# Kernel tuning notes

Hardware: AMD Instinct MI355X
Metric: run time of the kernel (lower is better)

Reference implementation:

```python
import jax, jax.numpy as jnp
import numpy as np

B, C, H, W, L = 2, 64, 48, 48, 48
GH, GW, GL = 24, 24, 24  # gating signal at half resolution


def setup_inputs() -> dict:
    key = jax.random.key(0)
    k = jax.random.split(key, 6)
    x = jax.random.normal(k[0], (B, C, H, W, L), dtype=jnp.float32)
    g = jax.random.normal(k[1], (B, C, GH, GW, GL), dtype=jnp.float32)
    s = 1.0 / np.sqrt(C)
    W1 = jax.random.normal(k[2], (C, C), dtype=jnp.float32) * s  # conv1 1x1x1 weight (out,in)
    b1 = jax.random.normal(k[3], (C,), dtype=jnp.float32) * 0.01
    W2 = jax.random.normal(k[4], (C, C), dtype=jnp.float32) * s  # conv2 1x1x1 weight
    b2 = jax.random.normal(k[5], (C,), dtype=jnp.float32) * 0.01
    return {"x": x, "g": g, "W1": W1, "b1": b1, "W2": W2, "b2": b2}


def _conv1x1(v, Wm, b):
    # 1x1x1 Conv3d == channel-mixing matmul
    return jnp.einsum('bchwl,oc->bohwl', v, Wm) + b[None, :, None, None, None]


def reference(x, g, W1, b1, W2, b2):
    theta_x = _conv1x1(x, W1, b1)                       # (B, C, H, W, L)
    theta_g = _conv1x1(g, W2, b2)                       # (B, C, GH, GW, GL)
    # F.upsample(mode='trilinear', align_corners=False) -> half-pixel trilinear resize
    theta_g = jax.image.resize(theta_g, (B, C, H, W, L), method='trilinear')

    # spatially-normalized elementwise gate
    theta_c = theta_x * theta_g
    theta_c = theta_c - jnp.min(theta_c)                # global min over whole tensor
    theta_c = theta_c / jnp.sum(theta_c, axis=(2, 3, 4), keepdims=True)
    p = theta_c * x

    # channel-channel attention per (b,h,w), contracting over L
    theta_c_d = jnp.einsum('bihwl,bjhwl->bhwij', theta_x, theta_g)  # (B,H,W,C,C)
    theta_c_d = theta_c_d - jnp.min(theta_c_d)
    theta_c_d = theta_c_d / jnp.sum(theta_c_d, axis=(1, 2, 3, 4), keepdims=True)
    d = jnp.einsum('bchwl,bhwcj->bjhwl', x, theta_c_d)  # (B, C, H, W, L)
    return (p, d)
```

## Files before the change

### kernel.cpp

```cpp
#include <hip/hip_runtime.h>

#define Bb 2
#define Cc 64
#define Hh 48
#define Ww 48
#define Ll 48
#define HWc (Hh*Ww)
#define HWL (HWc*Ll)
#define GHh 24
#define SG (GHh*GHh*GHh)
#define NBLK (Bb*HWc)
#define CNT1f 110592.0f
#define CNT2f 9437184.0f

__device__ __forceinline__ void interp1(int i, int& a, int& b, float& f){
  float src = i*0.5f - 0.25f;
  float fl = floorf(src);
  f = src - fl;
  int i0 = (int)fl;
  a = i0 < 0 ? 0 : i0;
  int i1 = i0 + 1;
  b = i1 > (GHh-1) ? (GHh-1) : i1;
}

__global__ __launch_bounds__(256) void conv_k(const float* __restrict__ in,
    const float* __restrict__ Wm, const float* __restrict__ bias,
    float* __restrict__ out, int S){
  __shared__ __align__(16) float Wl[64][68];
  __shared__ __align__(16) float xl[64][68];
  int t = threadIdx.x;
  int ntile = S >> 6;
  int b  = blockIdx.x / ntile;
  int s0 = (blockIdx.x % ntile) << 6;
  for (int q = t; q < 4096; q += 256){
    int o = q >> 6, c = q & 63;
    Wl[c][o] = Wm[q];
  }
  const float* inb = in + (size_t)b*Cc*S + s0;
  for (int q = t; q < 1024; q += 256){
    int c = q >> 4, v = (q & 15) << 2;
    float4 val = *(const float4*)(inb + (size_t)c*S + v);
    *(float4*)&xl[c][v] = val;
  }
  __syncthreads();
  int o0 = (t & 15) << 2, s1 = (t >> 4) << 2;
  float a00=0,a01=0,a02=0,a03=0,a10=0,a11=0,a12=0,a13=0;
  float a20=0,a21=0,a22=0,a23=0,a30=0,a31=0,a32=0,a33=0;
  #pragma unroll 8
  for (int c = 0; c < 64; ++c){
    float4 wv = *(const float4*)&Wl[c][o0];
    float4 xv = *(const float4*)&xl[c][s1];
    a00 += wv.x*xv.x; a01 += wv.x*xv.y; a02 += wv.x*xv.z; a03 += wv.x*xv.w;
    a10 += wv.y*xv.x; a11 += wv.y*xv.y; a12 += wv.y*xv.z; a13 += wv.y*xv.w;
    a20 += wv.z*xv.x; a21 += wv.z*xv.y; a22 += wv.z*xv.z; a23 += wv.z*xv.w;
    a30 += wv.w*xv.x; a31 += wv.w*xv.y; a32 += wv.w*xv.z; a33 += wv.w*xv.w;
  }
  float* ob = out + (size_t)b*Cc*S + s0 + s1;
  float b0 = bias[o0+0], b1v = bias[o0+1], b2v = bias[o0+2], b3 = bias[o0+3];
  { float4 r = make_float4(a00+b0,a01+b0,a02+b0,a03+b0); *(float4*)(ob + (size_t)(o0+0)*S) = r; }
  { float4 r = make_float4(a10+b1v,a11+b1v,a12+b1v,a13+b1v); *(float4*)(ob + (size_t)(o0+1)*S) = r; }
  { float4 r = make_float4(a20+b2v,a21+b2v,a22+b2v,a23+b2v); *(float4*)(ob + (size_t)(o0+2)*S) = r; }
  { float4 r = make_float4(a30+b3,a31+b3,a32+b3,a33+b3); *(float4*)(ob + (size_t)(o0+3)*S) = r; }
}

__global__ __launch_bounds__(256) void reduce_k(const float* __restrict__ tx,
    const float* __restrict__ tgh, float* __restrict__ tgsite,
    float* __restrict__ part_row, float* __restrict__ pm1,
    float* __restrict__ pm2, float* __restrict__ ps2){
  __shared__ __align__(16) float txt[64*52];
  __shared__ __align__(16) float tgt[64*52];
  __shared__ float Msh[64*25];
  __shared__ float red[512];
  __shared__ float sxg[48];
  int t = threadIdx.x;
  int bIdx = blockIdx.x;
  int b = bIdx / HWc, hw = bIdx % HWc;
  int h = hw / Ww, w = hw % Ww;
  int ha, hb; float fh; interp1(h, ha, hb, fh);
  int wa, wb; float fw; interp1(w, wa, wb, fw);
  float omh = 1.f - fh, omw = 1.f - fw;
  const float* txb = tx + ((size_t)b*Cc*HWc + hw)*Ll;
  #pragma unroll
  for (int k = 0; k < 3; ++k){
    int q = t + (k << 8);
    int c = q / 12, v = (q % 12) << 2;
    *(float4*)&txt[c*52+v] = *(const float4*)(txb + (size_t)c*HWL + v);
  }
  const float* gb = tgh + (size_t)b*Cc*SG;
  #pragma unroll
  for (int k = 0; k < 6; ++k){
    int q = t + (k << 8);
    int c = q / 24, j = q % 24;
    const float* gc = gb + (size_t)c*SG;
    float vaa = gc[ha*576 + wa*24 + j];
    float vba = gc[hb*576 + wa*24 + j];
    float vab = gc[ha*576 + wb*24 + j];
    float vbb = gc[hb*576 + wb*24 + j];
    float mwa = omh*vaa + fh*vba;
    float mwb = omh*vab + fh*vbb;
    Msh[c*25 + j] = omw*mwa + fw*mwb;
  }
  __syncthreads();
  float* tgs = tgsite + (size_t)bIdx*3072;
  #pragma unroll
  for (int k = 0; k < 3; ++k){
    int q = t + (k << 8);
    int c = q / 12, l4 = (q % 12) << 2;
    float4 r;
    float* rp = &r.x;
    #pragma unroll
    for (int i = 0; i < 4; ++i){
      int l = l4 + i;
      int la, lb; float fl; interp1(l, la, lb, fl);
      rp[i] = (1.f-fl)*Msh[c*25+la] + fl*Msh[c*25+lb];
    }
    *(float4*)&tgt[c*52+l4] = r;
    *(float4*)(tgs + c*48 + l4) = r;
  }
  __syncthreads();
  int c = t & 63, lq = t >> 6;
  float psum = 0.f, pmin = 3.4e38f;
  #pragma unroll
  for (int m = 0; m < 3; ++m){
    int l4 = (lq << 2) + (m << 4);
    float4 a = *(const float4*)&txt[c*52+l4];
    float4 g = *(const float4*)&tgt[c*52+l4];
    float p0 = a.x*g.x, p1 = a.y*g.y, p2 = a.z*g.z, p3 = a.w*g.w;
    psum += p0+p1+p2+p3;
    pmin = fminf(pmin, fminf(fminf(p0,p1), fminf(p2,p3)));
  }
  red[t] = psum;
  if (t < 48){
    float sx = 0.f, sg = 0.f;
    #pragma unroll 8
    for (int cc = 0; cc < 64; ++cc){ sx += txt[cc*52+t]; sg += tgt[cc*52+t]; }
    sxg[t] = sx*sg;
  }
  int i0 = (t & 15) << 2, j0 = (t >> 4) << 2;
  float a00=0,a01=0,a02=0,a03=0,a10=0,a11=0,a12=0,a13=0;
  float a20=0,a21=0,a22=0,a23=0,a30=0,a31=0,a32=0,a33=0;
  #pragma unroll 4
  for (int l0 = 0; l0 < 48; l0 += 4){
    float4 x0 = *(const float4*)&txt[(i0+0)*52 + l0];
    float4 x1 = *(const float4*)&txt[(i0+1)*52 + l0];
    float4 x2 = *(const float4*)&txt[(i0+2)*52 + l0];
    float4 x3 = *(const float4*)&txt[(i0+3)*52 + l0];
    float4 g0 = *(const float4*)&tgt[(j0+0)*52 + l0];
    float4 g1 = *(const float4*)&tgt[(j0+1)*52 + l0];
    float4 g2 = *(const float4*)&tgt[(j0+2)*52 + l0];
    float4 g3 = *(const float4*)&tgt[(j0+3)*52 + l0];
    a00 += x0.x*g0.x + x0.y*g0.y + x0.z*g0.z + x0.w*g0.w;
    a01 += x0.x*g1.x + x0.y*g1.y + x0.z*g1.z + x0.w*g1.w;
    a02 += x0.x*g2.x + x0.y*g2.y + x0.z*g2.z + x0.w*g2.w;
    a03 += x0.x*g3.x + x0.y*g3.y + x0.z*g3.z + x0.w*g3.w;
    a10 += x1.x*g0.x + x1.y*g0.y + x1.z*g0.z + x1.w*g0.w;
    a11 += x1.x*g1.x + x1.y*g1.y + x1.z*g1.z + x1.w*g1.w;
    a12 += x1.x*g2.x + x1.y*g2.y + x1.z*g2.z + x1.w*g2.w;
    a13 += x1.x*g3.x + x1.y*g3.y + x1.z*g3.z + x1.w*g3.w;
    a20 += x2.x*g0.x + x2.y*g0.y + x2.z*g0.z + x2.w*g0.w;
    a21 += x2.x*g1.x + x2.y*g1.y + x2.z*g1.z + x2.w*g1.w;
    a22 += x2.x*g2.x + x2.y*g2.y + x2.z*g2.z + x2.w*g2.w;
    a23 += x2.x*g3.x + x2.y*g3.y + x2.z*g3.z + x2.w*g3.w;
    a30 += x3.x*g0.x + x3.y*g0.y + x3.z*g0.z + x3.w*g0.w;
    a31 += x3.x*g1.x + x3.y*g1.y + x3.z*g1.z + x3.w*g1.w;
    a32 += x3.x*g2.x + x3.y*g2.y + x3.z*g2.z + x3.w*g2.w;
    a33 += x3.x*g3.x + x3.y*g3.y + x3.z*g3.z + x3.w*g3.w;
  }
  float amin = fminf(fminf(fminf(a00,a01),fminf(a02,a03)),
               fminf(fminf(fminf(a10,a11),fminf(a12,a13)),
               fminf(fminf(fminf(a20,a21),fminf(a22,a23)),
                     fminf(fminf(a30,a31),fminf(a32,a33)))));
  __syncthreads();
  if (t < 64) part_row[(size_t)bIdx*64 + t] = red[t]+red[t+64]+red[t+128]+red[t+192];
  __syncthreads();
  red[t] = pmin; red[256+t] = amin;
  __syncthreads();
  if (t < 128){
    red[t] = fminf(red[t], red[t+128]);
    red[256+t] = fminf(red[256+t], red[384+t]);
  }
  __syncthreads();
  if (t < 64){
    float v1 = fminf(red[t], red[t+64]);
    float v2 = fminf(red[256+t], red[320+t]);
    #pragma unroll
    for (int off = 32; off; off >>= 1){
      v1 = fminf(v1, __shfl_down(v1, off));
      v2 = fminf(v2, __shfl_down(v2, off));
    }
    if (t == 0){
      pm1[bIdx] = v1; pm2[bIdx] = v2;
      float tot = 0.f;
      #pragma unroll
      for (int l = 0; l < 48; ++l) tot += sxg[l];
      ps2[bIdx] = tot;
    }
  }
}

__global__ __launch_bounds__(256) void reduce2_k(const float* __restrict__ part_row,
    const float* __restrict__ pm1, const float* __restrict__ pm2,
    const float* __restrict__ ps2, float* __restrict__ rowsum,
    float* __restrict__ gmin, float* __restrict__ s2v){
  __shared__ float red[512];
  int t = threadIdx.x, blk = blockIdx.x;
  if (blk < 128){
    int b = blk >> 6, c = blk & 63;
    const float* src = part_row + (size_t)b*HWc*64 + c;
    float s = 0.f;
    #pragma unroll
    for (int k = 0; k < 9; ++k){
      int i = t + (k << 8);
      s += src[(size_t)i*64];
    }
    red[t] = s; __syncthreads();
    for (int sgap = 128; sgap >= 64; sgap >>= 1){
      if (t < sgap) red[t] += red[t+sgap];
      __syncthreads();
    }
    if (t < 64){
      float v = red[t];
      #pragma unroll
      for (int off = 32; off; off >>= 1) v += __shfl_down(v, off);
      if (t == 0) rowsum[blk] = v;
    }
  } else if (blk == 128){
    float m1 = 3.4e38f, m2 = 3.4e38f;
    for (int i = t; i < NBLK; i += 256){ m1 = fminf(m1, pm1[i]); m2 = fminf(m2, pm2[i]); }
    red[t] = m1; red[256+t] = m2; __syncthreads();
    for (int s = 128; s >= 1; s >>= 1){
      if (t < s){ red[t] = fminf(red[t], red[t+s]); red[256+t] = fminf(red[256+t], red[256+t+s]); }
      __syncthreads();
    }
    if (t == 0){ gmin[0] = red[0]; gmin[1] = red[256]; }
  } else {
    float sa = 0.f, sb = 0.f;
    for (int i = t; i < HWc; i += 256){ sa += ps2[i]; sb += ps2[HWc + i]; }
    red[t] = sa; red[256+t] = sb; __syncthreads();
    for (int s = 128; s >= 1; s >>= 1){
      if (t < s){ red[t] += red[t+s]; red[256+t] += red[256+t+s]; }
      __syncthreads();
    }
    if (t == 0){ s2v[0] = red[0]; s2v[1] = red[256]; }
  }
}

__global__ __launch_bounds__(256) void final_k(const float* __restrict__ x,
    const float* __restrict__ tx, const float* __restrict__ tgsite,
    const float* __restrict__ gmin, const float* __restrict__ rowsum,
    const float* __restrict__ s2v, float* __restrict__ outp, float* __restrict__ outd){
  __shared__ __align__(16) float txt[64*52];
  __shared__ __align__(16) float tgt[64*52];
  __shared__ __align__(16) float xs[64*52];
  __shared__ float iv1[64];
  int t = threadIdx.x;
  int bIdx = blockIdx.x;
  int b = bIdx / HWc, hw = bIdx % HWc;
  size_t sbase = ((size_t)b*Cc*HWc + hw)*Ll;
  const float* txb = tx + sbase;
  const float* xb  = x  + sbase;
  const float* tgs = tgsite + (size_t)bIdx*3072;
  float m1 = gmin[0], m2 = gmin[1];
  #pragma unroll
  for (int k = 0; k < 3; ++k){
    int q = t + (k << 8);
    int c = q / 12, v = (q % 12) << 2;
    *(float4*)&txt[c*52+v] = *(const float4*)(txb + (size_t)c*HWL + v);
    *(float4*)&xs [c*52+v] = *(const float4*)(xb  + (size_t)c*HWL + v);
    *(float4*)&tgt[c*52+v] = *(const float4*)(tgs + (q << 2));
  }
  if (t < 64) iv1[t] = 1.f/(rowsum[b*64 + t] - m1*CNT1f);
  float invd2 = 1.f/(s2v[b] - m2*CNT2f);
  __syncthreads();
  int i0 = (t & 15) << 2, j0 = (t >> 4) << 2;
  float a00=0,a01=0,a02=0,a03=0,a10=0,a11=0,a12=0,a13=0;
  float a20=0,a21=0,a22=0,a23=0,a30=0,a31=0,a32=0,a33=0;
  #pragma unroll 4
  for (int l0 = 0; l0 < 48; l0 += 4){
    float4 x0 = *(const float4*)&txt[(i0+0)*52 + l0];
    float4 x1 = *(const float4*)&txt[(i0+1)*52 + l0];
    float4 x2 = *(const float4*)&txt[(i0+2)*52 + l0];
    float4 x3 = *(const float4*)&txt[(i0+3)*52 + l0];
    float4 g0 = *(const float4*)&tgt[(j0+0)*52 + l0];
    float4 g1 = *(const float4*)&tgt[(j0+1)*52 + l0];
    float4 g2 = *(const float4*)&tgt[(j0+2)*52 + l0];
    float4 g3 = *(const float4*)&tgt[(j0+3)*52 + l0];
    a00 += x0.x*g0.x + x0.y*g0.y + x0.z*g0.z + x0.w*g0.w;
    a01 += x0.x*g1.x + x0.y*g1.y + x0.z*g1.z + x0.w*g1.w;
    a02 += x0.x*g2.x + x0.y*g2.y + x0.z*g2.z + x0.w*g2.w;
    a03 += x0.x*g3.x + x0.y*g3.y + x0.z*g3.z + x0.w*g3.w;
    a10 += x1.x*g0.x + x1.y*g0.y + x1.z*g0.z + x1.w*g0.w;
    a11 += x1.x*g1.x + x1.y*g1.y + x1.z*g1.z + x1.w*g1.w;
    a12 += x1.x*g2.x + x1.y*g2.y + x1.z*g2.z + x1.w*g2.w;
    a13 += x1.x*g3.x + x1.y*g3.y + x1.z*g3.z + x1.w*g3.w;
    a20 += x2.x*g0.x + x2.y*g0.y + x2.z*g0.z + x2.w*g0.w;
    a21 += x2.x*g1.x + x2.y*g1.y + x2.z*g1.z + x2.w*g1.w;
    a22 += x2.x*g2.x + x2.y*g2.y + x2.z*g2.z + x2.w*g2.w;
    a23 += x2.x*g3.x + x2.y*g3.y + x2.z*g3.z + x2.w*g3.w;
    a30 += x3.x*g0.x + x3.y*g0.y + x3.z*g0.z + x3.w*g0.w;
    a31 += x3.x*g1.x + x3.y*g1.y + x3.z*g1.z + x3.w*g1.w;
    a32 += x3.x*g2.x + x3.y*g2.y + x3.z*g2.z + x3.w*g2.w;
    a33 += x3.x*g3.x + x3.y*g3.y + x3.z*g3.z + x3.w*g3.w;
  }
  #pragma unroll
  for (int k = 0; k < 3; ++k){
    int q = t + (k << 8);
    int c = q / 12, l4 = (q % 12) << 2;
    float4 a = *(const float4*)&txt[c*52+l4];
    float4 g = *(const float4*)&tgt[c*52+l4];
    float4 xv = *(const float4*)&xs[c*52+l4];
    float s = iv1[c];
    float4 r = make_float4((a.x*g.x - m1)*s*xv.x, (a.y*g.y - m1)*s*xv.y,
                           (a.z*g.z - m1)*s*xv.z, (a.w*g.w - m1)*s*xv.w);
    *(float4*)(outp + sbase + (size_t)c*HWL + l4) = r;
  }
  __syncthreads();
  float* At = txt;
  { float4 r = make_float4((a00-m2)*invd2,(a01-m2)*invd2,(a02-m2)*invd2,(a03-m2)*invd2);
    *(float4*)&At[(i0+0)*52 + j0] = r; }
  { float4 r = make_float4((a10-m2)*invd2,(a11-m2)*invd2,(a12-m2)*invd2,(a13-m2)*invd2);
    *(float4*)&At[(i0+1)*52 + j0] = r; }
  { float4 r = make_float4((a20-m2)*invd2,(a21-m2)*invd2,(a22-m2)*invd2,(a23-m2)*invd2);
    *(float4*)&At[(i0+2)*52 + j0] = r; }
  { float4 r = make_float4((a30-m2)*invd2,(a31-m2)*invd2,(a32-m2)*invd2,(a33-m2)*invd2);
    *(float4*)&At[(i0+3)*52 + j0] = r; }
  __syncthreads();
  if (t < 192){
    int jj = (t & 15) << 2, l0 = (t >> 4) << 2;
    float d00=0,d01=0,d02=0,d03=0,d10=0,d11=0,d12=0,d13=0;
    float d20=0,d21=0,d22=0,d23=0,d30=0,d31=0,d32=0,d33=0;
    #pragma unroll 4
    for (int cc = 0; cc < 64; ++cc){
      float4 av = *(const float4*)&At[cc*52 + jj];
      float4 xv = *(const float4*)&xs[cc*52 + l0];
      d00 += av.x*xv.x; d01 += av.x*xv.y; d02 += av.x*xv.z; d03 += av.x*xv.w;
      d10 += av.y*xv.x; d11 += av.y*xv.y; d12 += av.y*xv.z; d13 += av.y*xv.w;
      d20 += av.z*xv.x; d21 += av.z*xv.y; d22 += av.z*xv.z; d23 += av.z*xv.w;
      d30 += av.w*xv.x; d31 += av.w*xv.y; d32 += av.w*xv.z; d33 += av.w*xv.w;
    }
    { float4 r = make_float4(d00,d01,d02,d03);
      *(float4*)(outd + sbase + (size_t)(jj+0)*HWL + l0) = r; }
    { float4 r = make_float4(d10,d11,d12,d13);
      *(float4*)(outd + sbase + (size_t)(jj+1)*HWL + l0) = r; }
    { float4 r = make_float4(d20,d21,d22,d23);
      *(float4*)(outd + sbase + (size_t)(jj+2)*HWL + l0) = r; }
    { float4 r = make_float4(d30,d31,d32,d33);
      *(float4*)(outd + sbase + (size_t)(jj+3)*HWL + l0) = r; }
  }
}

extern "C" void kernel_launch(void* const* d_in, const int* in_sizes, int n_in,
                              void* d_out, int out_size, void* d_ws, size_t ws_size,
                              hipStream_t stream){
  (void)in_sizes; (void)n_in; (void)out_size; (void)ws_size;
  const float* x  = (const float*)d_in[0];
  const float* g  = (const float*)d_in[1];
  const float* W1 = (const float*)d_in[2];
  const float* b1 = (const float*)d_in[3];
  const float* W2 = (const float*)d_in[4];
  const float* b2 = (const float*)d_in[5];
  float* outp = (float*)d_out;
  float* outd = outp + (size_t)Bb*Cc*HWL;
  float* ws   = (float*)d_ws;
  float* txw    = ws;
  float* tghw   = txw + (size_t)Bb*Cc*HWL;
  float* tgsite = tghw + (size_t)Bb*Cc*SG;
  float* part_row = tgsite + (size_t)Bb*Cc*HWL;
  float* pm1 = part_row + (size_t)NBLK*64;
  float* pm2 = pm1 + NBLK;
  float* ps2 = pm2 + NBLK;
  float* rowsum = ps2 + NBLK;
  float* gmin = rowsum + 128;
  float* s2v  = gmin + 2;

  hipLaunchKernelGGL(conv_k, dim3(Bb*(SG/64)), dim3(256), 0, stream, g, W2, b2, tghw, SG);
  hipLaunchKernelGGL(conv_k, dim3(Bb*(HWL/64)), dim3(256), 0, stream, x, W1, b1, txw, HWL);
  hipLaunchKernelGGL(reduce_k, dim3(NBLK), dim3(256), 0, stream, txw, tghw, tgsite,
                     part_row, pm1, pm2, ps2);
  hipLaunchKernelGGL(reduce2_k, dim3(130), dim3(256), 0, stream, part_row, pm1, pm2, ps2,
                     rowsum, gmin, s2v);
  hipLaunchKernelGGL(final_k, dim3(NBLK), dim3(256), 0, stream, x, txw, tgsite,
                     gmin, rowsum, s2v, outp, outd);
}
```

Before: 330.9 us.

## Fold L-axis trilinear upsample into theta_x to shrink channel-attention contraction

```diff
diff --git a/kernel.cpp b/kernel.cpp
--- a/kernel.cpp
+++ b/kernel.cpp
@@ -63,15 +63,34 @@
   { float4 r = make_float4(a30+b3,a31+b3,a32+b3,a33+b3); *(float4*)(ob + (size_t)(o0+3)*S) = r; }
 }
 
+__device__ __forceinline__ void g_fold(const float* __restrict__ txt,
+    float* __restrict__ G, int t){
+  int c = t >> 2, kb = (t & 3)*6;
+  const float* T = &txt[c*52];
+  #pragma unroll
+  for (int i = 0; i < 6; ++i){
+    int k = kb + i;
+    float v;
+    if (k == 0)       v = T[0] + 0.75f*T[1] + 0.25f*T[2];
+    else if (k == 23) v = 0.25f*T[45] + 0.75f*T[46] + T[47];
+    else              v = 0.25f*T[2*k-1] + 0.75f*T[2*k]
+                        + 0.75f*T[2*k+1] + 0.25f*T[2*k+2];
+    G[k*68 + c] = v;
+  }
+}
+
 __global__ __launch_bounds__(256) void reduce_k(const float* __restrict__ tx,
-    const float* __restrict__ tgh, float* __restrict__ tgsite,
+    const float* __restrict__ tgh, float* __restrict__ msite,
     float* __restrict__ part_row, float* __restrict__ pm1,
     float* __restrict__ pm2, float* __restrict__ ps2){
-  __shared__ __align__(16) float txt[64*52];
-  __shared__ __align__(16) float tgt[64*52];
-  __shared__ float Msh[64*25];
-  __shared__ float red[512];
-  __shared__ float sxg[48];
+  __shared__ __align__(16) float sh[7224];
+  float* txt = sh;
+  float* M   = sh + 3328;
+  float* G   = sh + 4960;
+  float* red = sh + 6592;
+  float* sxg = sh + 7104;
+  float* CM  = sh + 7152;
+  float* SX  = sh + 7176;
   int t = threadIdx.x;
   int bIdx = blockIdx.x;
   int b = bIdx / HWc, hw = bIdx % HWc;
@@ -87,84 +106,70 @@
     *(float4*)&txt[c*52+v] = *(const float4*)(txb + (size_t)c*HWL + v);
   }
   const float* gb = tgh + (size_t)b*Cc*SG;
-  #pragma unroll
-  for (int k = 0; k < 6; ++k){
-    int q = t + (k << 8);
-    int c = q / 24, j = q % 24;
+  for (int u = t; u < 384; u += 256){
+    int c = u / 6, s4 = (u % 6) << 2;
     const float* gc = gb + (size_t)c*SG;
-    float vaa = gc[ha*576 + wa*24 + j];
-    float vba = gc[hb*576 + wa*24 + j];
-    float vab = gc[ha*576 + wb*24 + j];
-    float vbb = gc[hb*576 + wb*24 + j];
-    float mwa = omh*vaa + fh*vba;
-    float mwb = omh*vab + fh*vbb;
-    Msh[c*25 + j] = omw*mwa + fw*mwb;
-  }
-  __syncthreads();
-  float* tgs = tgsite + (size_t)bIdx*3072;
-  #pragma unroll
-  for (int k = 0; k < 3; ++k){
-    int q = t + (k << 8);
-    int c = q / 12, l4 = (q % 12) << 2;
-    float4 r;
-    float* rp = &r.x;
-    #pragma unroll
-    for (int i = 0; i < 4; ++i){
-      int l = l4 + i;
-      int la, lb; float fl; interp1(l, la, lb, fl);
-      rp[i] = (1.f-fl)*Msh[c*25+la] + fl*Msh[c*25+lb];
-    }
-    *(float4*)&tgt[c*52+l4] = r;
-    *(float4*)(tgs + c*48 + l4) = r;
-  }
-  __syncthreads();
-  int c = t & 63, lq = t >> 6;
+    float4 vaa = *(const float4*)(gc + ha*576 + wa*24 + s4);
+    float4 vba = *(const float4*)(gc + hb*576 + wa*24 + s4);
+    float4 vab = *(const float4*)(gc + ha*576 + wb*24 + s4);
+    float4 vbb = *(const float4*)(gc + hb*576 + wb*24 + s4);
+    M[(s4+0)*68 + c] = omw*(omh*vaa.x + fh*vba.x) + fw*(omh*vab.x + fh*vbb.x);
+    M[(s4+1)*68 + c] = omw*(omh*vaa.y + fh*vba.y) + fw*(omh*vab.y + fh*vbb.y);
+    M[(s4+2)*68 + c] = omw*(omh*vaa.z + fh*vba.z) + fw*(omh*vab.z + fh*vbb.z);
+    M[(s4+3)*68 + c] = omw*(omh*vaa.w + fh*vba.w) + fw*(omh*vab.w + fh*vbb.w);
+  }
+  __syncthreads();
+  g_fold(txt, G, t);
+  if (t < 24){
+    float s = 0.f;
+    #pragma unroll 8
+    for (int c = 0; c < 64; ++c) s += M[t*68 + c];
+    CM[t] = s;
+  }
+  if (t >= 192 && t < 240){
+    int l = t - 192;
+    float s = 0.f;
+    #pragma unroll 8
+    for (int c = 0; c < 64; ++c) s += txt[c*52 + l];
+    SX[l] = s;
+  }
+  __syncthreads();
+  int c = t & 63, lg = t >> 6;
   float psum = 0.f, pmin = 3.4e38f;
-  #pragma unroll
-  for (int m = 0; m < 3; ++m){
-    int l4 = (lq << 2) + (m << 4);
-    float4 a = *(const float4*)&txt[c*52+l4];
-    float4 g = *(const float4*)&tgt[c*52+l4];
-    float p0 = a.x*g.x, p1 = a.y*g.y, p2 = a.z*g.z, p3 = a.w*g.w;
-    psum += p0+p1+p2+p3;
-    pmin = fminf(pmin, fminf(fminf(p0,p1), fminf(p2,p3)));
+  const float* Trow = &txt[c*52];
+  #pragma unroll
+  for (int li = 0; li < 12; ++li){
+    int l = lg*12 + li;
+    int la, lb; float fl; interp1(l, la, lb, fl);
+    float tgv = (1.f-fl)*M[la*68 + c] + fl*M[lb*68 + c];
+    float prod = Trow[l]*tgv;
+    psum += prod;
+    pmin = fminf(pmin, prod);
   }
   red[t] = psum;
   if (t < 48){
-    float sx = 0.f, sg = 0.f;
-    #pragma unroll 8
-    for (int cc = 0; cc < 64; ++cc){ sx += txt[cc*52+t]; sg += tgt[cc*52+t]; }
-    sxg[t] = sx*sg;
+    int la, lb; float fl; interp1(t, la, lb, fl);
+    sxg[t] = SX[t] * ((1.f-fl)*CM[la] + fl*CM[lb]);
+  }
+  float* msb = msite + (size_t)bIdx*1536;
+  for (int u = t; u < 384; u += 256){
+    int k = u >> 4, c4 = (u & 15) << 2;
+    float4 mv;
+    mv.x = M[k*68+c4+0]; mv.y = M[k*68+c4+1];
+    mv.z = M[k*68+c4+2]; mv.w = M[k*68+c4+3];
+    *(float4*)(msb + (u << 2)) = mv;
   }
   int i0 = (t & 15) << 2, j0 = (t >> 4) << 2;
   float a00=0,a01=0,a02=0,a03=0,a10=0,a11=0,a12=0,a13=0;
   float a20=0,a21=0,a22=0,a23=0,a30=0,a31=0,a32=0,a33=0;
   #pragma unroll 4
-  for (int l0 = 0; l0 < 48; l0 += 4){
-    float4 x0 = *(const float4*)&txt[(i0+0)*52 + l0];
-    float4 x1 = *(const float4*)&txt[(i0+1)*52 + l0];
-    float4 x2 = *(const float4*)&txt[(i0+2)*52 + l0];
-    float4 x3 = *(const float4*)&txt[(i0+3)*52 + l0];
-    float4 g0 = *(const float4*)&tgt[(j0+0)*52 + l0];
-    float4 g1 = *(const float4*)&tgt[(j0+1)*52 + l0];
-    float4 g2 = *(const float4*)&tgt[(j0+2)*52 + l0];
-    float4 g3 = *(const float4*)&tgt[(j0+3)*52 + l0];
-    a00 += x0.x*g0.x + x0.y*g0.y + x0.z*g0.z + x0.w*g0.w;
-    a01 += x0.x*g1.x + x0.y*g1.y + x0.z*g1.z + x0.w*g1.w;
-    a02 += x0.x*g2.x + x0.y*g2.y + x0.z*g2.z + x0.w*g2.w;
-    a03 += x0.x*g3.x + x0.y*g3.y + x0.z*g3.z + x0.w*g3.w;
-    a10 += x1.x*g0.x + x1.y*g0.y + x1.z*g0.z + x1.w*g0.w;
-    a11 += x1.x*g1.x + x1.y*g1.y + x1.z*g1.z + x1.w*g1.w;
-    a12 += x1.x*g2.x + x1.y*g2.y + x1.z*g2.z + x1.w*g2.w;
-    a13 += x1.x*g3.x + x1.y*g3.y + x1.z*g3.z + x1.w*g3.w;
-    a20 += x2.x*g0.x + x2.y*g0.y + x2.z*g0.z + x2.w*g0.w;
-    a21 += x2.x*g1.x + x2.y*g1.y + x2.z*g1.z + x2.w*g1.w;
-    a22 += x2.x*g2.x + x2.y*g2.y + x2.z*g2.z + x2.w*g2.w;
-    a23 += x2.x*g3.x + x2.y*g3.y + x2.z*g3.z + x2.w*g3.w;
-    a30 += x3.x*g0.x + x3.y*g0.y + x3.z*g0.z + x3.w*g0.w;
-    a31 += x3.x*g1.x + x3.y*g1.y + x3.z*g1.z + x3.w*g1.w;
-    a32 += x3.x*g2.x + x3.y*g2.y + x3.z*g2.z + x3.w*g2.w;
-    a33 += x3.x*g3.x + x3.y*g3.y + x3.z*g3.z + x3.w*g3.w;
+  for (int k = 0; k < 24; ++k){
+    float4 gv = *(const float4*)&G[k*68 + i0];
+    float4 mv = *(const float4*)&M[k*68 + j0];
+    a00 += gv.x*mv.x; a01 += gv.x*mv.y; a02 += gv.x*mv.z; a03 += gv.x*mv.w;
+    a10 += gv.y*mv.x; a11 += gv.y*mv.y; a12 += gv.y*mv.z; a13 += gv.y*mv.w;
+    a20 += gv.z*mv.x; a21 += gv.z*mv.y; a22 += gv.z*mv.z; a23 += gv.z*mv.w;
+    a30 += gv.w*mv.x; a31 += gv.w*mv.y; a32 += gv.w*mv.z; a33 += gv.w*mv.w;
   }
   float amin = fminf(fminf(fminf(a00,a01),fminf(a02,a03)),
                fminf(fminf(fminf(a10,a11),fminf(a12,a13)),
@@ -246,20 +251,21 @@
 }
 
 __global__ __launch_bounds__(256) void final_k(const float* __restrict__ x,
-    const float* __restrict__ tx, const float* __restrict__ tgsite,
+    const float* __restrict__ tx, const float* __restrict__ msite,
     const float* __restrict__ gmin, const float* __restrict__ rowsum,
     const float* __restrict__ s2v, float* __restrict__ outp, float* __restrict__ outd){
-  __shared__ __align__(16) float txt[64*52];
-  __shared__ __align__(16) float tgt[64*52];
-  __shared__ __align__(16) float xs[64*52];
-  __shared__ float iv1[64];
+  __shared__ __align__(16) float sh[9984];
+  float* txt = sh;
+  float* xs  = sh + 3328;
+  float* M   = sh + 6656;
+  float* G   = sh + 8288;
+  float* iv1 = sh + 9920;
   int t = threadIdx.x;
   int bIdx = blockIdx.x;
   int b = bIdx / HWc, hw = bIdx % HWc;
   size_t sbase = ((size_t)b*Cc*HWc + hw)*Ll;
   const float* txb = tx + sbase;
   const float* xb  = x  + sbase;
-  const float* tgs = tgsite + (size_t)bIdx*3072;
   float m1 = gmin[0], m2 = gmin[1];
   #pragma unroll
   for (int k = 0; k < 3; ++k){
@@ -267,51 +273,58 @@
     int c = q / 12, v = (q % 12) << 2;
     *(float4*)&txt[c*52+v] = *(const float4*)(txb + (size_t)c*HWL + v);
     *(float4*)&xs [c*52+v] = *(const float4*)(xb  + (size_t)c*HWL + v);
-    *(float4*)&tgt[c*52+v] = *(const float4*)(tgs + (q << 2));
+  }
+  const float* msb = msite + (size_t)bIdx*1536;
+  for (int u = t; u < 384; u += 256){
+    float4 mv = *(const float4*)(msb + (u << 2));
+    int k = u >> 4, c4 = (u & 15) << 2;
+    *(float4*)&M[k*68 + c4] = mv;
   }
   if (t < 64) iv1[t] = 1.f/(rowsum[b*64 + t] - m1*CNT1f);
   float invd2 = 1.f/(s2v[b] - m2*CNT2f);
+  __syncthreads();
+  g_fold(txt, G, t);
   __syncthreads();
   int i0 = (t & 15) << 2, j0 = (t >> 4) << 2;
   float a00=0,a01=0,a02=0,a03=0,a10=0,a11=0,a12=0,a13=0;
   float a20=0,a21=0,a22=0,a23=0,a30=0,a31=0,a32=0,a33=0;
   #pragma unroll 4
-  for (int l0 = 0; l0 < 48; l0 += 4){
-    float4 x0 = *(const float4*)&txt[(i0+0)*52 + l0];
-    float4 x1 = *(const float4*)&txt[(i0+1)*52 + l0];
-    float4 x2 = *(const float4*)&txt[(i0+2)*52 + l0];
-    float4 x3 = *(const float4*)&txt[(i0+3)*52 + l0];
-    float4 g0 = *(const float4*)&tgt[(j0+0)*52 + l0];
-    float4 g1 = *(const float4*)&tgt[(j0+1)*52 + l0];
-    float4 g2 = *(const float4*)&tgt[(j0+2)*52 + l0];
-    float4 g3 = *(const float4*)&tgt[(j0+3)*52 + l0];
-    a00 += x0.x*g0.x + x0.y*g0.y + x0.z*g0.z + x0.w*g0.w;
-    a01 += x0.x*g1.x + x0.y*g1.y + x0.z*g1.z + x0.w*g1.w;
-    a02 += x0.x*g2.x + x0.y*g2.y + x0.z*g2.z + x0.w*g2.w;
-    a03 += x0.x*g3.x + x0.y*g3.y + x0.z*g3.z + x0.w*g3.w;
-    a10 += x1.x*g0.x + x1.y*g0.y + x1.z*g0.z + x1.w*g0.w;
-    a11 += x1.x*g1.x + x1.y*g1.y + x1.z*g1.z + x1.w*g1.w;
-    a12 += x1.x*g2.x + x1.y*g2.y + x1.z*g2.z + x1.w*g2.w;
-    a13 += x1.x*g3.x + x1.y*g3.y + x1.z*g3.z + x1.w*g3.w;
-    a20 += x2.x*g0.x + x2.y*g0.y + x2.z*g0.z + x2.w*g0.w;
-    a21 += x2.x*g1.x + x2.y*g1.y + x2.z*g1.z + x2.w*g1.w;
-    a22 += x2.x*g2.x + x2.y*g2.y + x2.z*g2.z + x2.w*g2.w;
-    a23 += x2.x*g3.x + x2.y*g3.y + x2.z*g3.z + x2.w*g3.w;
-    a30 += x3.x*g0.x + x3.y*g0.y + x3.z*g0.z + x3.w*g0.w;
-    a31 += x3.x*g1.x + x3.y*g1.y + x3.z*g1.z + x3.w*g1.w;
-    a32 += x3.x*g2.x + x3.y*g2.y + x3.z*g2.z + x3.w*g2.w;
-    a33 += x3.x*g3.x + x3.y*g3.y + x3.z*g3.z + x3.w*g3.w;
+  for (int k = 0; k < 24; ++k){
+    float4 gv = *(const float4*)&G[k*68 + i0];
+    float4 mv = *(const float4*)&M[k*68 + j0];
+    a00 += gv.x*mv.x; a01 += gv.x*mv.y; a02 += gv.x*mv.z; a03 += gv.x*mv.w;
+    a10 += gv.y*mv.x; a11 += gv.y*mv.y; a12 += gv.y*mv.z; a13 += gv.y*mv.w;
+    a20 += gv.z*mv.x; a21 += gv.z*mv.y; a22 += gv.z*mv.z; a23 += gv.z*mv.w;
+    a30 += gv.w*mv.x; a31 += gv.w*mv.y; a32 += gv.w*mv.z; a33 += gv.w*mv.w;
   }
   #pragma unroll
   for (int k = 0; k < 3; ++k){
     int q = t + (k << 8);
     int c = q / 12, l4 = (q % 12) << 2;
-    float4 a = *(const float4*)&txt[c*52+l4];
-    float4 g = *(const float4*)&tgt[c*52+l4];
-    float4 xv = *(const float4*)&xs[c*52+l4];
+    float4 a  = *(const float4*)&txt[c*52+l4];
+    float4 xv = *(const float4*)&xs [c*52+l4];
     float s = iv1[c];
-    float4 r = make_float4((a.x*g.x - m1)*s*xv.x, (a.y*g.y - m1)*s*xv.y,
-                           (a.z*g.z - m1)*s*xv.z, (a.w*g.w - m1)*s*xv.w);
+    float4 r;
+    {
+      int la, lb; float fl; interp1(l4+0, la, lb, fl);
+      float tgv = (1.f-fl)*M[la*68+c] + fl*M[lb*68+c];
+      r.x = (a.x*tgv - m1)*s*xv.x;
+    }
+    {
+      int la, lb; float fl; interp1(l4+1, la, lb, fl);
+      float tgv = (1.f-fl)*M[la*68+c] + fl*M[lb*68+c];
+      r.y = (a.y*tgv - m1)*s*xv.y;
+    }
+    {
+      int la, lb; float fl; interp1(l4+2, la, lb, fl);
+      float tgv = (1.f-fl)*M[la*68+c] + fl*M[lb*68+c];
+      r.z = (a.z*tgv - m1)*s*xv.z;
+    }
+    {
+      int la, lb; float fl; interp1(l4+3, la, lb, fl);
+      float tgv = (1.f-fl)*M[la*68+c] + fl*M[lb*68+c];
+      r.w = (a.w*tgv - m1)*s*xv.w;
+    }
     *(float4*)(outp + sbase + (size_t)c*HWL + l4) = r;
   }
   __syncthreads();
@@ -364,8 +377,8 @@
   float* ws   = (float*)d_ws;
   float* txw    = ws;
   float* tghw   = txw + (size_t)Bb*Cc*HWL;
-  float* tgsite = tghw + (size_t)Bb*Cc*SG;
-  float* part_row = tgsite + (size_t)Bb*Cc*HWL;
+  float* msite  = tghw + (size_t)Bb*Cc*SG;
+  float* part_row = msite + (size_t)NBLK*1536;
   float* pm1 = part_row + (size_t)NBLK*64;
   float* pm2 = pm1 + NBLK;
   float* ps2 = pm2 + NBLK;
@@ -375,10 +388,10 @@
 
   hipLaunchKernelGGL(conv_k, dim3(Bb*(SG/64)), dim3(256), 0, stream, g, W2, b2, tghw, SG);
   hipLaunchKernelGGL(conv_k, dim3(Bb*(HWL/64)), dim3(256), 0, stream, x, W1, b1, txw, HWL);
-  hipLaunchKernelGGL(reduce_k, dim3(NBLK), dim3(256), 0, stream, txw, tghw, tgsite,
+  hipLaunchKernelGGL(reduce_k, dim3(NBLK), dim3(256), 0, stream, txw, tghw, msite,
                      part_row, pm1, pm2, ps2);
   hipLaunchKernelGGL(reduce2_k, dim3(130), dim3(256), 0, stream, part_row, pm1, pm2, ps2,
                      rowsum, gmin, s2v);
-  hipLaunchKernelGGL(final_k, dim3(NBLK), dim3(256), 0, stream, x, txw, tgsite,
+  hipLaunchKernelGGL(final_k, dim3(NBLK), dim3(256), 0, stream, x, txw, msite,
                      gmin, rowsum, s2v, outp, outd);
 }
```

Result: faster. 306.3 us (-7.4%).
